# Performance work log

Hardware: AMD Instinct MI355X
Metric: run time of the kernel (lower is better)

## Reference

```python
import jax, jax.numpy as jnp
import numpy as np

NUM_HEADS = 12
HEAD_DIM = 64
HIDDEN = NUM_HEADS * HEAD_DIM  # 768


def setup_inputs() -> dict:
    key = jax.random.key(0)
    ks = jax.random.split(key, 18)
    B, Ni, Nt, H = 8, 1024, 512, HIDDEN
    inp = {
        "hidden_states": jax.random.normal(ks[0], (B, Ni, H), jnp.float32),
        "text": jax.random.normal(ks[1], (B, Nt, H), jnp.float32),
    }
    names = ["Wq", "Wk", "Wv", "Wqt", "Wkt", "Wvt", "Wo"]
    for i, n in enumerate(names):
        inp[n] = jax.random.normal(ks[2 + i], (H, H), jnp.float32) * 0.02
        inp["b" + n[1:]] = jnp.zeros((H,), jnp.float32)
    return inp


def _split_heads(x):
    # [B, S, H] -> [B, h, S, dh]
    B, S, _ = x.shape
    return x.reshape(B, S, NUM_HEADS, HEAD_DIM).transpose(0, 2, 1, 3)


def _merge_heads(x):
    # [B, h, S, dh] -> [B, S, H]
    B, h, S, dh = x.shape
    return x.transpose(0, 2, 1, 3).reshape(B, S, h * dh)


def _attend(q, k, v):
    scale = 1.0 / jnp.sqrt(jnp.asarray(HEAD_DIM, q.dtype))
    scores = jnp.einsum("bhqd,bhkd->bhqk", q, k) * scale
    probs = jax.nn.softmax(scores, axis=-1)
    ctx = jnp.einsum("bhqk,bhkd->bhqd", probs, v)
    return ctx, probs


def reference(hidden_states, text, Wq, bq, Wk, bk, Wv, bv,
              Wqt, bqt, Wkt, bkt, Wvt, bvt, Wo, bo):
    q_i = _split_heads(hidden_states @ Wq + bq)
    k_i = _split_heads(hidden_states @ Wk + bk)
    v_i = _split_heads(hidden_states @ Wv + bv)
    q_t = _split_heads(text @ Wqt + bqt)
    k_t = _split_heads(text @ Wkt + bkt)
    v_t = _split_heads(text @ Wvt + bvt)

    ctx_ii, weights = _attend(q_i, k_i, v_i)   # img -> img (weights returned, vis=True)
    ctx_tt, _ = _attend(q_t, k_t, v_t)         # text -> text
    ctx_it, _ = _attend(q_i, k_t, v_t)         # img queries, text keys/values
    ctx_ti, _ = _attend(q_t, k_i, v_i)         # text queries, img keys/values

    out_img = (_merge_heads(ctx_ii) + _merge_heads(ctx_it)) * 0.5 @ Wo + bo
    out_text = (_merge_heads(ctx_tt) + _merge_heads(ctx_ti)) * 0.5 @ Wo + bo
    return out_img, out_text, weights
```

## Files before the change

kernel.cpp:

```cpp
#include <hip/hip_runtime.h>

typedef __attribute__((ext_vector_type(4))) float f32x4;
typedef __attribute__((ext_vector_type(8))) short short8;
typedef __attribute__((ext_vector_type(4))) unsigned short us4;
typedef unsigned short u16;
typedef unsigned char uchar;

__device__ __forceinline__ u16 f2b(float f) {
  union { float f; unsigned u; } a; a.f = f;
  unsigned r = a.u + 0x7fffu + ((a.u >> 16) & 1u);
  return (u16)(r >> 16);
}
__device__ __forceinline__ unsigned cvtpk2(float lo, float hi) {
  unsigned r;
  asm("v_cvt_pk_bf16_f32 %0, %1, %2" : "=v"(r) : "v"(lo), "v"(hi));
  return r;
}
__device__ __forceinline__ short8 cvt8(f32x4 a, f32x4 b) {
  union { unsigned u[4]; short8 s; } r;
  r.u[0] = cvtpk2(a[0], a[1]); r.u[1] = cvtpk2(a[2], a[3]);
  r.u[2] = cvtpk2(b[0], b[1]); r.u[3] = cvtpk2(b[2], b[3]);
  return r.s;
}
#define SWZ(r, byteoff) ((((r) * 128) + (byteoff)) ^ (((r) & 7) << 4))

typedef __attribute__((address_space(1))) const void* gp1;
typedef __attribute__((address_space(3))) void* lp3;
__device__ __forceinline__ void gload16(const void* g, void* lds_wave_uniform_base) {
  __builtin_amdgcn_global_load_lds((gp1)g, (lp3)lds_wave_uniform_base, 16, 0, 0);
}

__global__ __launch_bounds__(256) void prep_kernel(
    const float* w0, const float* w1, const float* w2, const float* w3,
    const float* w4, const float* w5, const float* w6, u16* wt,
    const float* __restrict__ h, const float* __restrict__ tx, u16* __restrict__ xb)
{
  const int bid = blockIdx.x, t = threadIdx.x;
  if (bid < 1008) {
    __shared__ float tile[64][65];
    const float* Ws[7] = {w0, w1, w2, w3, w4, w5, w6};
    int z = bid / 144, rem = bid % 144;
    const float* W = Ws[z];
    u16* out = wt + (size_t)z * 589824;
    const int r0 = (rem / 12) * 64, c0 = (rem % 12) * 64;
#pragma unroll
    for (int i = 0; i < 4; ++i) {
      int idx = i * 256 + t;
      int r = idx >> 4, c = (idx & 15) * 4;
      f32x4 v = *(const f32x4*)(W + (size_t)(r0 + r) * 768 + (c0 + c));
      tile[r][c + 0] = v[0]; tile[r][c + 1] = v[1];
      tile[r][c + 2] = v[2]; tile[r][c + 3] = v[3];
    }
    __syncthreads();
#pragma unroll
    for (int i = 0; i < 4; ++i) {
      int idx = i * 256 + t;
      int rn = idx >> 4, c = (idx & 15) * 4;
      union { us4 o; unsigned u[2]; } o;
      o.u[0] = cvtpk2(tile[c + 0][rn], tile[c + 1][rn]);
      o.u[1] = cvtpk2(tile[c + 2][rn], tile[c + 3][rn]);
      *(us4*)(out + (size_t)(c0 + rn) * 768 + (r0 + c)) = o.o;
    }
  } else {
    size_t e = ((size_t)(bid - 1008) * 256 + t) * 8;
    const float* src; size_t off;
    if (e < 6291456) { src = h; off = e; } else { src = tx; off = e - 6291456; }
    f32x4 v0 = *(const f32x4*)(src + off), v1 = *(const f32x4*)(src + off + 4);
    *(short8*)(xb + e) = cvt8(v0, v1);
  }
}

__global__ __launch_bounds__(256) void proj_kernel(
    const u16* __restrict__ Xb, const u16* __restrict__ wt,
    const float* __restrict__ bq, const float* __restrict__ bk, const float* __restrict__ bv,
    const float* __restrict__ bqt, const float* __restrict__ bkt, const float* __restrict__ bvt,
    u16* __restrict__ qi, u16* __restrict__ ki, u16* __restrict__ vti,
    u16* __restrict__ qt, u16* __restrict__ ktx, u16* __restrict__ vtt)
{
  const int bid = blockIdx.x;
  const int wk = (bid & 7) * 216 + (bid >> 3);
  const bool img = wk < 1152;
  const int id = img ? wk : wk - 1152;
  const int y = img ? (id >> 6) : (id >> 5);
  const int x = img ? (id & 63) : (id & 31);
  const int z = y / 6, n0 = (y % 6) * 128, m0 = x * 128;
  const int S = img ? 1024 : 512, logS = img ? 10 : 9;
  const u16* X = img ? Xb : Xb + 6291456;
  const u16* Wt = wt + (img ? 0 : (size_t)3 * 589824) + (size_t)y * 98304;
  const float* bias = img ? (z == 0 ? bq : z == 1 ? bk : bv)
                          : (z == 0 ? bqt : z == 1 ? bkt : bvt);
  u16* out = img ? (z == 0 ? qi : z == 1 ? ki : vti)
                 : (z == 0 ? qt : z == 1 ? ktx : vtt);
  const bool vmode = (z == 2);
  __shared__ unsigned char sm[36864];
  unsigned char* Asm = sm;
  unsigned char* Bsm = sm + 16384;
  const int t = threadIdx.x, w = t >> 6, l = t & 63;
  const int wm = (w & 1) * 64, wn = (w >> 1) * 64;
  f32x4 acc[4][4] = {};
  for (int k0 = 0; k0 < 768; k0 += 64) {
#pragma unroll
    for (int j = 0; j < 4; ++j) {
      int chunk = j * 4 + w;
      int r = chunk * 8 + (l >> 3);
      int cb = ((l & 7) * 16) ^ ((r & 7) << 4);
      gload16(X + (size_t)(m0 + r) * 768 + k0 + cb / 2, Asm + chunk * 1024);
    }
#pragma unroll
    for (int j = 0; j < 4; ++j) {
      int chunk = j * 4 + w;
      int r = chunk * 8 + (l >> 3);
      int cb = ((l & 7) * 16) ^ ((r & 7) << 4);
      gload16(Wt + (size_t)r * 768 + k0 + cb / 2, Bsm + chunk * 1024);
    }
    __syncthreads();
#pragma unroll
    for (int kc = 0; kc < 2; ++kc) {
      short8 af[4], bfr[4];
      const int koff = (kc * 32 + (l >> 4) * 8) * 2;
#pragma unroll
      for (int ms = 0; ms < 4; ++ms) {
        int row = wm + ms * 16 + (l & 15);
        af[ms] = *(const short8*)(Asm + SWZ(row, koff));
      }
#pragma unroll
      for (int ns = 0; ns < 4; ++ns) {
        int row = wn + ns * 16 + (l & 15);
        bfr[ns] = *(const short8*)(Bsm + SWZ(row, koff));
      }
      __builtin_amdgcn_s_setprio(1);
#pragma unroll
      for (int ms = 0; ms < 4; ++ms)
#pragma unroll
        for (int ns = 0; ns < 4; ++ns)
          acc[ms][ns] = __builtin_amdgcn_mfma_f32_16x16x32_bf16(af[ms], bfr[ns], acc[ms][ns], 0, 0, 0);
      __builtin_amdgcn_s_setprio(0);
    }
    __syncthreads();
  }
  float bvv[4];
#pragma unroll
  for (int ns = 0; ns < 4; ++ns) bvv[ns] = bias[n0 + wn + ns * 16 + (l & 15)];
#pragma unroll
  for (int ms = 0; ms < 4; ++ms)
#pragma unroll
    for (int ns = 0; ns < 4; ++ns)
#pragma unroll
      for (int i = 0; i < 4; ++i) {
        u16 u = f2b(acc[ms][ns][i] + bvv[ns]);
        int mm = wm + ms * 16 + (l >> 4) * 4 + i;
        int nn = wn + ns * 16 + (l & 15);
        int row = vmode ? nn : mm, col = vmode ? mm : nn;
        *(u16*)(sm + row * 272 + col * 2) = u;
      }
  __syncthreads();
  if (!vmode) {
#pragma unroll
    for (int i = 0; i < 8; ++i) {
      int idx = i * 256 + t;
      int r = idx >> 4, c = (idx & 15) * 8;
      short8 v = *(const short8*)(sm + r * 272 + c * 2);
      int sg = m0 + r, b = sg >> logS, s = sg & (S - 1);
      int n = n0 + c, hh = n >> 6, d = n & 63;
      *(short8*)(out + (((size_t)b * 12 + hh) * S + s) * 64 + d) = v;
    }
  } else {
#pragma unroll
    for (int i = 0; i < 8; ++i) {
      int idx = i * 256 + t;
      int r = idx >> 4, c = (idx & 15) * 8;
      short8 v = *(const short8*)(sm + r * 272 + c * 2);
      int n = n0 + r, hh = n >> 6, d = n & 63;
      int sg = m0 + c, b = sg >> logS, s = sg & (S - 1);
      *(short8*)(out + (((size_t)b * 12 + hh) * 64 + d) * S + s) = v;
    }
  }
}

__device__ __forceinline__ void stage_k(const u16* Kp, int kt, uchar* Ksm, int w, int l) {
#pragma unroll
  for (int j = 0; j < 2; ++j) {
    int chunk = j * 4 + w;
    int r = chunk * 8 + (l >> 3);
    int cb = ((l & 7) * 16) ^ ((r & 7) << 4);
    gload16(Kp + (size_t)(kt * 64 + r) * 64 + cb / 2, Ksm + chunk * 1024);
  }
}
__device__ __forceinline__ void stage_v(const u16* Vp, int kt, int Sk, uchar* Vsm, int w, int l) {
#pragma unroll
  for (int j = 0; j < 2; ++j) {
    int chunk = j * 4 + w;
    int r = chunk * 8 + (l >> 3);
    int cb = ((l & 7) * 16) ^ ((r & 7) << 4);
    gload16(Vp + (size_t)r * Sk + kt * 64 + cb / 2, Vsm + chunk * 1024);
  }
}
__device__ __forceinline__ void kfrags(const uchar* Ksm, int l, short8 kf[8]) {
#pragma unroll
  for (int kc = 0; kc < 2; ++kc)
#pragma unroll
    for (int sub = 0; sub < 4; ++sub) {
      int row = sub * 16 + (l & 15);
      kf[kc * 4 + sub] = *(const short8*)(Ksm + SWZ(row, (kc * 32 + (l >> 4) * 8) * 2));
    }
}
__device__ __forceinline__ void vfrags(const uchar* Vsm, int l, short8 vb[8]) {
#pragma unroll
  for (int ds = 0; ds < 4; ++ds) {
    int row = ds * 16 + (l & 15);
    vb[ds * 2]     = *(const short8*)(Vsm + SWZ(row, ((l >> 4) * 8) * 2));
    vb[ds * 2 + 1] = *(const short8*)(Vsm + SWZ(row, (32 + (l >> 4) * 8) * 2));
  }
}
__device__ __forceinline__ void qk_mfma2(const short8 qf[2][2], const short8 kf[8], f32x4 sfr[2][4]) {
  __builtin_amdgcn_s_setprio(1);
#pragma unroll
  for (int m = 0; m < 2; ++m)
#pragma unroll
    for (int kc = 0; kc < 2; ++kc)
#pragma unroll
      for (int sub = 0; sub < 4; ++sub)
        sfr[m][sub] = __builtin_amdgcn_mfma_f32_16x16x32_bf16(qf[m][kc], kf[kc * 4 + sub], sfr[m][sub], 0, 0, 0);
  __builtin_amdgcn_s_setprio(0);
}
__device__ __forceinline__ void pv8v(const uchar* Pf, const short8 vb[8], int l, f32x4 og[4]) {
  const uchar* base = Pf + (l & 15) * 272 + (l >> 4) * 32;
  f32x4 a0 = *(const f32x4*)(base);
  f32x4 a1 = *(const f32x4*)(base + 16);
  f32x4 b0 = *(const f32x4*)(base + 128);
  f32x4 b1 = *(const f32x4*)(base + 144);
  short8 pa0 = cvt8(a0, a1), pa1 = cvt8(b0, b1);
  __builtin_amdgcn_s_setprio(1);
#pragma unroll
  for (int ds = 0; ds < 4; ++ds) {
    og[ds] = __builtin_amdgcn_mfma_f32_16x16x32_bf16(pa0, vb[ds * 2], og[ds], 0, 0, 0);
    og[ds] = __builtin_amdgcn_mfma_f32_16x16x32_bf16(pa1, vb[ds * 2 + 1], og[ds], 0, 0, 0);
  }
  __builtin_amdgcn_s_setprio(0);
}
__device__ __forceinline__ void red16_2(float v[2][4]) {
#pragma unroll
  for (int d = 1; d < 16; d <<= 1)
#pragma unroll
    for (int m = 0; m < 2; ++m)
#pragma unroll
      for (int i = 0; i < 4; ++i) v[m][i] += __shfl_xor(v[m][i], d);
}
__device__ __forceinline__ void pass_unnorm(
    const u16* __restrict__ Kp, const u16* __restrict__ Vp, int Sk,
    const short8 qf[2][2], uchar* Ks0, uchar* Ks1, uchar* Vs0, uchar* Vs1, uchar* Pf,
    int w, int l, f32x4 og[2][4], float ll[2][4])
{
  const int nkt = Sk >> 6;
  stage_k(Kp, 0, Ks0, w, l);
  stage_v(Vp, 0, Sk, Vs0, w, l);
  __syncthreads();
  for (int kt = 0; kt < nkt; ++kt) {
    uchar* Kc = (kt & 1) ? Ks1 : Ks0;
    uchar* Vc = (kt & 1) ? Vs1 : Vs0;
    if (kt + 1 < nkt) {
      stage_k(Kp, kt + 1, (kt & 1) ? Ks0 : Ks1, w, l);
      stage_v(Vp, kt + 1, Sk, (kt & 1) ? Vs0 : Vs1, w, l);
    }
    short8 kf[8];
    kfrags(Kc, l, kf);
    f32x4 sfr[2][4] = {};
    qk_mfma2(qf, kf, sfr);
    short8 vb[8];
    vfrags(Vc, l, vb);
#pragma unroll
    for (int m = 0; m < 2; ++m) {
#pragma unroll
      for (int sub = 0; sub < 4; ++sub)
#pragma unroll
        for (int i = 0; i < 4; ++i) {
          float p = __expf(sfr[m][sub][i] * 0.125f);
          ll[m][i] += p;
          *(float*)(Pf + ((l >> 4) * 4 + i) * 272 + (sub * 16 + (l & 15)) * 4) = p;
        }
      pv8v(Pf, vb, l, og[m]);
    }
    __syncthreads();
  }
}

__global__ __launch_bounds__(256) void attn_kernel(
    const u16* __restrict__ qi, const u16* __restrict__ ki, const u16* __restrict__ vti,
    const u16* __restrict__ qt, const u16* __restrict__ ktx, const u16* __restrict__ vtt,
    u16* __restrict__ cimg, u16* __restrict__ ctxt, float* __restrict__ weights)
{
  __shared__ uchar smem[50176];
  const int t = threadIdx.x, w = t >> 6, l = t & 63;
  uchar* Ks0 = smem;
  uchar* Ks1 = smem + 8192;
  uchar* Vs0 = smem + 16384;
  uchar* Vs1 = smem + 24576;
  uchar* Pf  = smem + 32768 + w * 4352;

  const int bid = blockIdx.x;
  const int wk = (bid & 7) * 144 + (bid >> 3);
  const bool img = wk < 768;
  const int id = img ? wk : wk - 768;
  const int x = img ? (id & 7) : (id & 3);
  const int head = img ? (id >> 3) : (id >> 2);
  const int b = head / 12, h = head % 12;
  const int Sq = img ? 1024 : 512;
  const int SkA = img ? 1024 : 512, SkB = img ? 512 : 1024;
  const u16* Qp = (img ? qi : qt) + (size_t)head * Sq * 64;
  const u16* KpA = (img ? ki : ktx) + (size_t)head * SkA * 64;
  const u16* VpA = (img ? vti : vtt) + (size_t)head * 64 * SkA;
  const u16* KpB = (img ? ktx : ki) + (size_t)head * SkB * 64;
  const u16* VpB = (img ? vtt : vti) + (size_t)head * 64 * SkB;
  u16* CTX = img ? cimg : ctxt;
  float* PROBS = img ? weights : nullptr;
  const int q0 = x * 128;

  short8 qf[2][2];
#pragma unroll
  for (int m = 0; m < 2; ++m) {
    int row = q0 + m * 64 + w * 16 + (l & 15);
    qf[m][0] = *(const short8*)(Qp + (size_t)row * 64 + (l >> 4) * 8);
    qf[m][1] = *(const short8*)(Qp + (size_t)row * 64 + 32 + (l >> 4) * 8);
  }

  f32x4 of[2][4] = {};
  if (PROBS) {
    float ll[2][4] = {};
    const int nkt = SkA >> 6;
    stage_k(KpA, 0, Ks0, w, l);
    __syncthreads();
    for (int kt = 0; kt < nkt; ++kt) {
      uchar* Kc = (kt & 1) ? Ks1 : Ks0;
      if (kt + 1 < nkt) stage_k(KpA, kt + 1, (kt & 1) ? Ks0 : Ks1, w, l);
      short8 kf[8];
      kfrags(Kc, l, kf);
      f32x4 sfr[2][4] = {};
      qk_mfma2(qf, kf, sfr);
#pragma unroll
      for (int m = 0; m < 2; ++m)
#pragma unroll
        for (int sub = 0; sub < 4; ++sub)
#pragma unroll
          for (int i = 0; i < 4; ++i) ll[m][i] += __expf(sfr[m][sub][i] * 0.125f);
      __syncthreads();
    }
    stage_k(KpA, 0, Ks0, w, l);
    stage_v(VpA, 0, SkA, Vs0, w, l);
    red16_2(ll);
    float rl[2][4];
#pragma unroll
    for (int m = 0; m < 2; ++m)
#pragma unroll
      for (int i = 0; i < 4; ++i) rl[m][i] = 1.0f / ll[m][i];
    __syncthreads();
    for (int kt = 0; kt < nkt; ++kt) {
      uchar* Kc = (kt & 1) ? Ks1 : Ks0;
      uchar* Vc = (kt & 1) ? Vs1 : Vs0;
      if (kt + 1 < nkt) {
        stage_k(KpA, kt + 1, (kt & 1) ? Ks0 : Ks1, w, l);
        stage_v(VpA, kt + 1, SkA, (kt & 1) ? Vs0 : Vs1, w, l);
      }
      short8 kf[8];
      kfrags(Kc, l, kf);
      f32x4 sfr[2][4] = {};
      qk_mfma2(qf, kf, sfr);
      short8 vb[8];
      vfrags(Vc, l, vb);
#pragma unroll
      for (int m = 0; m < 2; ++m) {
#pragma unroll
        for (int sub = 0; sub < 4; ++sub)
#pragma unroll
          for (int i = 0; i < 4; ++i) {
            float p = __expf(sfr[m][sub][i] * 0.125f) * rl[m][i];
            *(float*)(Pf + ((l >> 4) * 4 + i) * 272 + (sub * 16 + (l & 15)) * 4) = p;
          }
        const size_t pbase = ((size_t)head * Sq + q0 + m * 64 + w * 16);
#pragma unroll
        for (int ps = 0; ps < 4; ++ps) {
          int row = ps * 4 + (l >> 4);
          f32x4 v = *(const f32x4*)(Pf + row * 272 + (l & 15) * 16);
          *(f32x4*)(PROBS + (pbase + row) * (size_t)SkA + kt * 64 + (l & 15) * 4) = v;
        }
        pv8v(Pf, vb, l, of[m]);
      }
      __syncthreads();
    }
#pragma unroll
    for (int m = 0; m < 2; ++m)
#pragma unroll
      for (int ds = 0; ds < 4; ++ds) of[m][ds] *= 0.5f;
  } else {
    float ll[2][4] = {};
    pass_unnorm(KpA, VpA, SkA, qf, Ks0, Ks1, Vs0, Vs1, Pf, w, l, of, ll);
    red16_2(ll);
#pragma unroll
    for (int m = 0; m < 2; ++m)
#pragma unroll
      for (int ds = 0; ds < 4; ++ds)
#pragma unroll
        for (int i = 0; i < 4; ++i) of[m][ds][i] *= 0.5f / ll[m][i];
  }
  {
    f32x4 og[2][4] = {};
    float l2[2][4] = {};
    pass_unnorm(KpB, VpB, SkB, qf, Ks0, Ks1, Vs0, Vs1, Pf, w, l, og, l2);
    red16_2(l2);
#pragma unroll
    for (int m = 0; m < 2; ++m)
#pragma unroll
      for (int ds = 0; ds < 4; ++ds)
#pragma unroll
        for (int i = 0; i < 4; ++i) of[m][ds][i] += og[m][ds][i] * (0.5f / l2[m][i]);
  }
#pragma unroll
  for (int m = 0; m < 2; ++m) {
#pragma unroll
    for (int ds = 0; ds < 4; ++ds)
#pragma unroll
      for (int i = 0; i < 4; ++i)
        *(float*)(Pf + ((l >> 4) * 4 + i) * 272 + (ds * 16 + (l & 15)) * 4) = of[m][ds][i];
#pragma unroll
    for (int i = 0; i < 2; ++i) {
      int it = i * 64 + l;
      int r = it >> 3, cg = it & 7;
      f32x4 v0 = *(const f32x4*)(Pf + r * 272 + cg * 32);
      f32x4 v1 = *(const f32x4*)(Pf + r * 272 + cg * 32 + 16);
      int s = q0 + m * 64 + w * 16 + r;
      *(short8*)(CTX + ((size_t)b * Sq + s) * 768 + h * 64 + cg * 8) = cvt8(v0, v1);
    }
  }
}

__global__ __launch_bounds__(256) void outproj_kernel(
    const u16* __restrict__ cimg, const u16* __restrict__ ctxt,
    const u16* __restrict__ Wto, const float* __restrict__ bias,
    float* __restrict__ out_img, float* __restrict__ out_text)
{
  const int bid = blockIdx.x;
  const int wk = (bid & 7) * 72 + (bid >> 3);
  const bool img = wk < 384;
  const int id = img ? wk : wk - 384;
  const int y = img ? (id >> 6) : (id >> 5);
  const int x = img ? (id & 63) : (id & 31);
  const u16* C = img ? cimg : ctxt;
  float* OUT = img ? out_img : out_text;
  const int m0 = x * 128, n0 = y * 128;
  __shared__ unsigned char sm[32768];
  unsigned char* Asm = sm;
  unsigned char* Bsm = sm + 16384;
  const int t = threadIdx.x, w = t >> 6, l = t & 63;
  const int wm = (w & 1) * 64, wn = (w >> 1) * 64;
  f32x4 acc[4][4] = {};
  for (int k0 = 0; k0 < 768; k0 += 64) {
#pragma unroll
    for (int j = 0; j < 4; ++j) {
      int chunk = j * 4 + w;
      int r = chunk * 8 + (l >> 3);
      int cb = ((l & 7) * 16) ^ ((r & 7) << 4);
      gload16(C + (size_t)(m0 + r) * 768 + k0 + cb / 2, Asm + chunk * 1024);
    }
#pragma unroll
    for (int j = 0; j < 4; ++j) {
      int chunk = j * 4 + w;
      int r = chunk * 8 + (l >> 3);
      int cb = ((l & 7) * 16) ^ ((r & 7) << 4);
      gload16(Wto + (size_t)(n0 + r) * 768 + k0 + cb / 2, Bsm + chunk * 1024);
    }
    __syncthreads();
#pragma unroll
    for (int kc = 0; kc < 2; ++kc) {
      short8 af[4], bfr[4];
      const int koff = (kc * 32 + (l >> 4) * 8) * 2;
#pragma unroll
      for (int ms = 0; ms < 4; ++ms) {
        int row = wm + ms * 16 + (l & 15);
        af[ms] = *(const short8*)(Asm + SWZ(row, koff));
      }
#pragma unroll
      for (int ns = 0; ns < 4; ++ns) {
        int row = wn + ns * 16 + (l & 15);
        bfr[ns] = *(const short8*)(Bsm + SWZ(row, koff));
      }
      __builtin_amdgcn_s_setprio(1);
#pragma unroll
      for (int ms = 0; ms < 4; ++ms)
#pragma unroll
        for (int ns = 0; ns < 4; ++ns)
          acc[ms][ns] = __builtin_amdgcn_mfma_f32_16x16x32_bf16(af[ms], bfr[ns], acc[ms][ns], 0, 0, 0);
      __builtin_amdgcn_s_setprio(0);
    }
    __syncthreads();
  }
#pragma unroll
  for (int ms = 0; ms < 4; ++ms)
#pragma unroll
    for (int ns = 0; ns < 4; ++ns) {
      float bv = bias[n0 + wn + ns * 16 + (l & 15)];
#pragma unroll
      for (int i = 0; i < 4; ++i) {
        int mm = m0 + wm + ms * 16 + (l >> 4) * 4 + i;
        int nn = n0 + wn + ns * 16 + (l & 15);
        OUT[(size_t)mm * 768 + nn] = acc[ms][ns][i] + bv;
      }
    }
}

extern "C" void kernel_launch(void* const* d_in, const int* in_sizes, int n_in,
                              void* d_out, int out_size, void* d_ws, size_t ws_size,
                              hipStream_t stream)
{
  const float* hidden = (const float*)d_in[0];
  const float* text   = (const float*)d_in[1];
  const float* Wq  = (const float*)d_in[2];  const float* bq  = (const float*)d_in[3];
  const float* Wk  = (const float*)d_in[4];  const float* bk  = (const float*)d_in[5];
  const float* Wv  = (const float*)d_in[6];  const float* bv  = (const float*)d_in[7];
  const float* Wqt = (const float*)d_in[8];  const float* bqt = (const float*)d_in[9];
  const float* Wkt = (const float*)d_in[10]; const float* bkt = (const float*)d_in[11];
  const float* Wvt = (const float*)d_in[12]; const float* bvt = (const float*)d_in[13];
  const float* Wo  = (const float*)d_in[14]; const float* bo  = (const float*)d_in[15];

  u16* wt   = (u16*)d_ws;
  u16* xb   = wt + 7 * 589824;
  u16* qi   = xb + 9437184;
  u16* ki   = qi + 6291456;
  u16* vti  = ki + 6291456;
  u16* qt   = vti + 6291456;
  u16* ktx  = qt + 3145728;
  u16* vtt  = ktx + 3145728;
  u16* cimg = vtt + 3145728;
  u16* ctxt = cimg + 6291456;

  float* out_img  = (float*)d_out;
  float* out_text = out_img + 6291456;
  float* weights  = out_text + 3145728;

  prep_kernel<<<5616, 256, 0, stream>>>(Wq, Wk, Wv, Wqt, Wkt, Wvt, Wo, wt,
                                        hidden, text, xb);
  proj_kernel<<<1728, 256, 0, stream>>>(xb, wt, bq, bk, bv, bqt, bkt, bvt,
                                        qi, ki, vti, qt, ktx, vtt);
  attn_kernel<<<1152, 256, 0, stream>>>(qi, ki, vti, qt, ktx, vtt,
                                        cimg, ctxt, weights);
  outproj_kernel<<<576, 256, 0, stream>>>(cimg, ctxt, wt + 6 * 589824, bo,
                                          out_img, out_text);
}
```

Baseline: 327.7 us.

## Compute transposed QK scores so P feeds PV MFMA directly from registers

The QK MFMA operands are swapped so each lane holds one query row's scores across keys. P can then be packed to bf16 in registers and fed straight into 16x16x16 MFMAs for the PV product, with no round trip through LDS. This removes the per-tile LDS writes and reads of P in the unnormalized passes, and the row-sum reduction becomes two cross-lane shuffles. In exchange, PV uses twice as many smaller MFMA instructions with 8-byte V fragment loads, and normalizing the output needs ds_bpermute to move row sums across lanes.

```diff
diff --git a/kernel.cpp b/kernel.cpp
--- a/kernel.cpp
+++ b/kernel.cpp
@@ -2,6 +2,7 @@
 
 typedef __attribute__((ext_vector_type(4))) float f32x4;
 typedef __attribute__((ext_vector_type(8))) short short8;
+typedef __attribute__((ext_vector_type(4))) short s16x4;
 typedef __attribute__((ext_vector_type(4))) unsigned short us4;
 typedef unsigned short u16;
 typedef unsigned char uchar;
@@ -21,6 +22,16 @@
   r.u[0] = cvtpk2(a[0], a[1]); r.u[1] = cvtpk2(a[2], a[3]);
   r.u[2] = cvtpk2(b[0], b[1]); r.u[3] = cvtpk2(b[2], b[3]);
   return r.s;
+}
+__device__ __forceinline__ f32x4 mfma16(s16x4 a, s16x4 b, f32x4 c) {
+#if __has_builtin(__builtin_amdgcn_mfma_f32_16x16x16bf16_1k)
+  return __builtin_amdgcn_mfma_f32_16x16x16bf16_1k(a, b, c, 0, 0, 0);
+#elif __has_builtin(__builtin_amdgcn_mfma_f32_16x16x16_bf16_1k)
+  return __builtin_amdgcn_mfma_f32_16x16x16_bf16_1k(a, b, c, 0, 0, 0);
+#else
+  asm("v_mfma_f32_16x16x16_bf16 %0, %1, %2, %0" : "+v"(c) : "v"(a), "v"(b));
+  return c;
+#endif
 }
 #define SWZ(r, byteoff) ((((r) * 128) + (byteoff)) ^ (((r) & 7) << 4))
 
@@ -204,15 +215,7 @@
       kf[kc * 4 + sub] = *(const short8*)(Ksm + SWZ(row, (kc * 32 + (l >> 4) * 8) * 2));
     }
 }
-__device__ __forceinline__ void vfrags(const uchar* Vsm, int l, short8 vb[8]) {
-#pragma unroll
-  for (int ds = 0; ds < 4; ++ds) {
-    int row = ds * 16 + (l & 15);
-    vb[ds * 2]     = *(const short8*)(Vsm + SWZ(row, ((l >> 4) * 8) * 2));
-    vb[ds * 2 + 1] = *(const short8*)(Vsm + SWZ(row, (32 + (l >> 4) * 8) * 2));
-  }
-}
-__device__ __forceinline__ void qk_mfma2(const short8 qf[2][2], const short8 kf[8], f32x4 sfr[2][4]) {
+__device__ __forceinline__ void qk_swapped(const short8 qf[2][2], const short8 kf[8], f32x4 sfr[2][4]) {
   __builtin_amdgcn_s_setprio(1);
 #pragma unroll
   for (int m = 0; m < 2; ++m)
@@ -220,36 +223,39 @@
     for (int kc = 0; kc < 2; ++kc)
 #pragma unroll
       for (int sub = 0; sub < 4; ++sub)
-        sfr[m][sub] = __builtin_amdgcn_mfma_f32_16x16x32_bf16(qf[m][kc], kf[kc * 4 + sub], sfr[m][sub], 0, 0, 0);
+        sfr[m][sub] = __builtin_amdgcn_mfma_f32_16x16x32_bf16(kf[kc * 4 + sub], qf[m][kc], sfr[m][sub], 0, 0, 0);
   __builtin_amdgcn_s_setprio(0);
 }
-__device__ __forceinline__ void pv8v(const uchar* Pf, const short8 vb[8], int l, f32x4 og[4]) {
-  const uchar* base = Pf + (l & 15) * 272 + (l >> 4) * 32;
-  f32x4 a0 = *(const f32x4*)(base);
-  f32x4 a1 = *(const f32x4*)(base + 16);
-  f32x4 b0 = *(const f32x4*)(base + 128);
-  f32x4 b1 = *(const f32x4*)(base + 144);
-  short8 pa0 = cvt8(a0, a1), pa1 = cvt8(b0, b1);
+__device__ __forceinline__ void pv16(const uchar* Vsm, const s16x4 pa[4], int l, f32x4 og[4]) {
+  s16x4 vb[16];
+#pragma unroll
+  for (int ds = 0; ds < 4; ++ds)
+#pragma unroll
+    for (int kk = 0; kk < 4; ++kk) {
+      int row = ds * 16 + (l & 15);
+      vb[ds * 4 + kk] = *(const s16x4*)(Vsm + SWZ(row, kk * 32 + (l >> 4) * 8));
+    }
   __builtin_amdgcn_s_setprio(1);
 #pragma unroll
-  for (int ds = 0; ds < 4; ++ds) {
-    og[ds] = __builtin_amdgcn_mfma_f32_16x16x32_bf16(pa0, vb[ds * 2], og[ds], 0, 0, 0);
-    og[ds] = __builtin_amdgcn_mfma_f32_16x16x32_bf16(pa1, vb[ds * 2 + 1], og[ds], 0, 0, 0);
-  }
+  for (int kk = 0; kk < 4; ++kk)
+#pragma unroll
+    for (int ds = 0; ds < 4; ++ds)
+      og[ds] = mfma16(pa[kk], vb[ds * 4 + kk], og[ds]);
   __builtin_amdgcn_s_setprio(0);
 }
-__device__ __forceinline__ void red16_2(float v[2][4]) {
-#pragma unroll
-  for (int d = 1; d < 16; d <<= 1)
-#pragma unroll
-    for (int m = 0; m < 2; ++m)
-#pragma unroll
-      for (int i = 0; i < 4; ++i) v[m][i] += __shfl_xor(v[m][i], d);
+__device__ __forceinline__ void pa_build(const float ps[16], s16x4 pa[4]) {
+#pragma unroll
+  for (int s = 0; s < 4; ++s) {
+    union { unsigned u[2]; s16x4 v; } r;
+    r.u[0] = cvtpk2(ps[s * 4 + 0], ps[s * 4 + 1]);
+    r.u[1] = cvtpk2(ps[s * 4 + 2], ps[s * 4 + 3]);
+    pa[s] = r.v;
+  }
 }
 __device__ __forceinline__ void pass_unnorm(
     const u16* __restrict__ Kp, const u16* __restrict__ Vp, int Sk,
-    const short8 qf[2][2], uchar* Ks0, uchar* Ks1, uchar* Vs0, uchar* Vs1, uchar* Pf,
-    int w, int l, f32x4 og[2][4], float ll[2][4])
+    const short8 qf[2][2], uchar* Ks0, uchar* Ks1, uchar* Vs0, uchar* Vs1,
+    int w, int l, f32x4 og[2][4], float ll[2])
 {
   const int nkt = Sk >> 6;
   stage_k(Kp, 0, Ks0, w, l);
@@ -265,20 +271,21 @@
     short8 kf[8];
     kfrags(Kc, l, kf);
     f32x4 sfr[2][4] = {};
-    qk_mfma2(qf, kf, sfr);
-    short8 vb[8];
-    vfrags(Vc, l, vb);
+    qk_swapped(qf, kf, sfr);
 #pragma unroll
     for (int m = 0; m < 2; ++m) {
+      float ps[16];
 #pragma unroll
       for (int sub = 0; sub < 4; ++sub)
 #pragma unroll
         for (int i = 0; i < 4; ++i) {
           float p = __expf(sfr[m][sub][i] * 0.125f);
-          ll[m][i] += p;
-          *(float*)(Pf + ((l >> 4) * 4 + i) * 272 + (sub * 16 + (l & 15)) * 4) = p;
+          ll[m] += p;
+          ps[sub * 4 + i] = p;
         }
-      pv8v(Pf, vb, l, og[m]);
+      s16x4 pa[4];
+      pa_build(ps, pa);
+      pv16(Vc, pa, l, og[m]);
     }
     __syncthreads();
   }
@@ -325,7 +332,7 @@
 
   f32x4 of[2][4] = {};
   if (PROBS) {
-    float ll[2][4] = {};
+    float ll[2] = {0.f, 0.f};
     const int nkt = SkA >> 6;
     stage_k(KpA, 0, Ks0, w, l);
     __syncthreads();
@@ -335,23 +342,24 @@
       short8 kf[8];
       kfrags(Kc, l, kf);
       f32x4 sfr[2][4] = {};
-      qk_mfma2(qf, kf, sfr);
+      qk_swapped(qf, kf, sfr);
 #pragma unroll
       for (int m = 0; m < 2; ++m)
 #pragma unroll
         for (int sub = 0; sub < 4; ++sub)
 #pragma unroll
-          for (int i = 0; i < 4; ++i) ll[m][i] += __expf(sfr[m][sub][i] * 0.125f);
+          for (int i = 0; i < 4; ++i) ll[m] += __expf(sfr[m][sub][i] * 0.125f);
       __syncthreads();
     }
     stage_k(KpA, 0, Ks0, w, l);
     stage_v(VpA, 0, SkA, Vs0, w, l);
-    red16_2(ll);
-    float rl[2][4];
-#pragma unroll
-    for (int m = 0; m < 2; ++m)
-#pragma unroll
-      for (int i = 0; i < 4; ++i) rl[m][i] = 1.0f / ll[m][i];
+    float rl[2];
+#pragma unroll
+    for (int m = 0; m < 2; ++m) {
+      ll[m] += __shfl_xor(ll[m], 16);
+      ll[m] += __shfl_xor(ll[m], 32);
+      rl[m] = 1.0f / ll[m];
+    }
     __syncthreads();
     for (int kt = 0; kt < nkt; ++kt) {
       uchar* Kc = (kt & 1) ? Ks1 : Ks0;
@@ -363,26 +371,28 @@
       short8 kf[8];
       kfrags(Kc, l, kf);
       f32x4 sfr[2][4] = {};
-      qk_mfma2(qf, kf, sfr);
-      short8 vb[8];
-      vfrags(Vc, l, vb);
+      qk_swapped(qf, kf, sfr);
 #pragma unroll
       for (int m = 0; m < 2; ++m) {
-#pragma unroll
-        for (int sub = 0; sub < 4; ++sub)
-#pragma unroll
-          for (int i = 0; i < 4; ++i) {
-            float p = __expf(sfr[m][sub][i] * 0.125f) * rl[m][i];
-            *(float*)(Pf + ((l >> 4) * 4 + i) * 272 + (sub * 16 + (l & 15)) * 4) = p;
-          }
+        float ps[16];
+#pragma unroll
+        for (int sub = 0; sub < 4; ++sub) {
+#pragma unroll
+          for (int i = 0; i < 4; ++i)
+            ps[sub * 4 + i] = __expf(sfr[m][sub][i] * 0.125f) * rl[m];
+          *(f32x4*)(Pf + (l & 15) * 272 + (sub * 16 + (l >> 4) * 4) * 4) =
+              *(const f32x4*)&ps[sub * 4];
+        }
         const size_t pbase = ((size_t)head * Sq + q0 + m * 64 + w * 16);
 #pragma unroll
-        for (int ps = 0; ps < 4; ++ps) {
-          int row = ps * 4 + (l >> 4);
+        for (int psr = 0; psr < 4; ++psr) {
+          int row = psr * 4 + (l >> 4);
           f32x4 v = *(const f32x4*)(Pf + row * 272 + (l & 15) * 16);
           *(f32x4*)(PROBS + (pbase + row) * (size_t)SkA + kt * 64 + (l & 15) * 4) = v;
         }
-        pv8v(Pf, vb, l, of[m]);
+        s16x4 pa[4];
+        pa_build(ps, pa);
+        pv16(Vc, pa, l, of[m]);
       }
       __syncthreads();
     }
@@ -391,27 +401,39 @@
 #pragma unroll
       for (int ds = 0; ds < 4; ++ds) of[m][ds] *= 0.5f;
   } else {
-    float ll[2][4] = {};
-    pass_unnorm(KpA, VpA, SkA, qf, Ks0, Ks1, Vs0, Vs1, Pf, w, l, of, ll);
-    red16_2(ll);
-#pragma unroll
-    for (int m = 0; m < 2; ++m)
-#pragma unroll
-      for (int ds = 0; ds < 4; ++ds)
-#pragma unroll
-        for (int i = 0; i < 4; ++i) of[m][ds][i] *= 0.5f / ll[m][i];
+    float ll[2] = {0.f, 0.f};
+    pass_unnorm(KpA, VpA, SkA, qf, Ks0, Ks1, Vs0, Vs1, w, l, of, ll);
+#pragma unroll
+    for (int m = 0; m < 2; ++m) {
+      ll[m] += __shfl_xor(ll[m], 16);
+      ll[m] += __shfl_xor(ll[m], 32);
+      float r = 0.5f / ll[m];
+#pragma unroll
+      for (int i = 0; i < 4; ++i) {
+        float lv = __int_as_float(__builtin_amdgcn_ds_bpermute(
+            ((l >> 4) * 4 + i) * 4, __float_as_int(r)));
+#pragma unroll
+        for (int ds = 0; ds < 4; ++ds) of[m][ds][i] *= lv;
+      }
+    }
   }
   {
     f32x4 og[2][4] = {};
-    float l2[2][4] = {};
-    pass_unnorm(KpB, VpB, SkB, qf, Ks0, Ks1, Vs0, Vs1, Pf, w, l, og, l2);
-    red16_2(l2);
-#pragma unroll
-    for (int m = 0; m < 2; ++m)
-#pragma unroll
-      for (int ds = 0; ds < 4; ++ds)
-#pragma unroll
-        for (int i = 0; i < 4; ++i) of[m][ds][i] += og[m][ds][i] * (0.5f / l2[m][i]);
+    float l2[2] = {0.f, 0.f};
+    pass_unnorm(KpB, VpB, SkB, qf, Ks0, Ks1, Vs0, Vs1, w, l, og, l2);
+#pragma unroll
+    for (int m = 0; m < 2; ++m) {
+      l2[m] += __shfl_xor(l2[m], 16);
+      l2[m] += __shfl_xor(l2[m], 32);
+      float r = 0.5f / l2[m];
+#pragma unroll
+      for (int i = 0; i < 4; ++i) {
+        float lv = __int_as_float(__builtin_amdgcn_ds_bpermute(
+            ((l >> 4) * 4 + i) * 4, __float_as_int(r)));
+#pragma unroll
+        for (int ds = 0; ds < 4; ++ds) of[m][ds][i] += og[m][ds][i] * lv;
+      }
+    }
   }
 #pragma unroll
   for (int m = 0; m < 2; ++m) {
```

Result: slower. 385.7 us (+17.7%).
